# Kernel optimization log

Measured on AMD Instinct MI355X. Metric: run time of the kernel, lower is better.

## Reference

```python
import jax, jax.numpy as jnp
import numpy as np

B, IN, HID, OUT = 1024, 512, 128, 64
INP1 = IN + 1  # 513, after prepending ones column


def setup_inputs() -> dict:
    key = jax.random.key(0)
    k1, k2, k3, k4, k5, k6, k7, k8 = jax.random.split(key, 8)
    s1 = 1.0 / np.sqrt(INP1 * INP1)
    s2 = 1.0 / np.sqrt(HID)
    return {
        "img": jax.random.normal(k1, (B, IN), dtype=jnp.float32),
        "tab": jax.random.normal(k2, (B, IN), dtype=jnp.float32),
        "W1": jax.random.uniform(k3, (HID, INP1 * INP1), jnp.float32, -s1, s1),
        "b1": jax.random.uniform(k4, (HID,), jnp.float32, -s1, s1),
        "W2": jax.random.uniform(k5, (HID, HID), jnp.float32, -s2, s2),
        "b2": jax.random.uniform(k6, (HID,), jnp.float32, -s2, s2),
        "W3": jax.random.uniform(k7, (OUT, HID), jnp.float32, -s2, s2),
        "b3": jax.random.uniform(k8, (OUT,), jnp.float32, -s2, s2),
    }


def reference(img, tab, W1, b1, W2, b2, W3, b3):
    ones = jnp.ones((img.shape[0], 1), dtype=img.dtype)
    x = jnp.concatenate([ones, img], axis=1)  # [B, IN+1]
    t = jnp.concatenate([ones, tab], axis=1)  # [B, IN+1]
    # batched outer product, flattened: [B, (IN+1)*(IN+1)]
    fusion = jnp.einsum("bi,bj->bij", x, t).reshape(x.shape[0], -1)
    # dropout is identity in eval mode
    y1 = fusion @ W1.T + b1
    y2 = jnp.tanh(y1 @ W2.T + b2)
    y3 = jax.nn.relu(y2 @ W3.T + b3)
    return y3
```

## Files before the change

kernel.cpp:

```cpp
#include <hip/hip_runtime.h>
#include <hip/hip_bf16.h>

typedef __bf16 bf16x8 __attribute__((ext_vector_type(8)));
typedef float f32x4 __attribute__((ext_vector_type(4)));

#define B_SZ   1024
#define IN_SZ  512
#define HID    128
#define OUT_SZ 64
#define KPAD   544
#define BM     64
#define BN     512
#define BK     32
#define NKT    (KPAD/BK)
#define APAD   40

static __device__ __forceinline__ unsigned short f2bf(float f) {
    __hip_bfloat16 h = __float2bfloat16(f);
    return *reinterpret_cast<unsigned short*>(&h);
}

__global__ __launch_bounds__(256) void prep_kernel(
    const float* __restrict__ img, const float* __restrict__ tab,
    unsigned short* __restrict__ tbt, float* __restrict__ xhT)
{
    const int blk = blockIdx.x;
    for (int j = threadIdx.x; j < KPAD; j += 256) {
        float v = (j == 0) ? 1.0f : (j < 513 ? tab[(size_t)blk * IN_SZ + (j - 1)] : 0.0f);
        tbt[(size_t)blk * KPAD + j] = f2bf(v);
    }
    if (blk < KPAD) {
        const int i = blk;
        for (int b = threadIdx.x; b < B_SZ; b += 256) {
            float v = (i == 0) ? 1.0f : (i < 513 ? img[(size_t)b * IN_SZ + (i - 1)] : 0.0f);
            xhT[(size_t)i * B_SZ + b] = v;
        }
    }
}

__global__ __launch_bounds__(512) void gemm_fused(
    const float* __restrict__ w1, const unsigned short* __restrict__ tbt,
    const float* __restrict__ xhT, float* __restrict__ y1acc)
{
    __shared__ unsigned short Als[BM][APAD];
    __shared__ unsigned short Bls[BN][APAD];

    const int bm = blockIdx.x >> 1;
    const int bn = blockIdx.x & 1;
    const int m0 = bm * BM;
    const int n0 = bn * BN;
    const int tid  = threadIdx.x;
    const int wv   = tid >> 6;
    const int lane = tid & 63;
    const int l15  = lane & 15;
    const int kg   = lane >> 4;

    const f32x4 zero4 = {0.f, 0.f, 0.f, 0.f};
    f32x4 acc[4][4];
    #pragma unroll
    for (int i = 0; i < 4; ++i)
        #pragma unroll
        for (int j = 0; j < 4; ++j) acc[i][j] = zero4;

    const int ar = tid >> 3;
    const int ac = (tid & 7) << 2;

    for (int kt = 0; kt < NKT; ++kt) {
        __syncthreads();
        {
            const int j0 = kt * BK + ac;
            const size_t gb = (size_t)(m0 + ar) * 513 + j0;
            unsigned short u0, u1, u2, u3;
            if (kt < NKT - 1) {
                u0 = f2bf(w1[gb + 0]); u1 = f2bf(w1[gb + 1]);
                u2 = f2bf(w1[gb + 2]); u3 = f2bf(w1[gb + 3]);
            } else {
                u0 = (j0 + 0 < 513) ? f2bf(w1[gb + 0]) : (unsigned short)0;
                u1 = (j0 + 1 < 513) ? f2bf(w1[gb + 1]) : (unsigned short)0;
                u2 = (j0 + 2 < 513) ? f2bf(w1[gb + 2]) : (unsigned short)0;
                u3 = (j0 + 3 < 513) ? f2bf(w1[gb + 3]) : (unsigned short)0;
            }
            Als[ar][ac + 0] = u0; Als[ar][ac + 1] = u1;
            Als[ar][ac + 2] = u2; Als[ar][ac + 3] = u3;
        }
        {
            const uint4* src = reinterpret_cast<const uint4*>(
                tbt + (size_t)(n0 + tid) * KPAD + kt * BK);
            uint4 v0 = src[0], v1 = src[1], v2 = src[2], v3 = src[3];
            uint4* dst = reinterpret_cast<uint4*>(&Bls[tid][0]);
            dst[0] = v0; dst[1] = v1; dst[2] = v2; dst[3] = v3;
        }
        __syncthreads();
        bf16x8 af[4], bfr[4];
        #pragma unroll
        for (int ms = 0; ms < 4; ++ms)
            af[ms] = *reinterpret_cast<const bf16x8*>(&Als[ms * 16 + l15][kg * 8]);
        #pragma unroll
        for (int ns = 0; ns < 4; ++ns)
            bfr[ns] = *reinterpret_cast<const bf16x8*>(&Bls[wv * 64 + ns * 16 + l15][kg * 8]);
        #pragma unroll
        for (int ms = 0; ms < 4; ++ms)
            #pragma unroll
            for (int ns = 0; ns < 4; ++ns)
                acc[ms][ns] = __builtin_amdgcn_mfma_f32_16x16x32_bf16(
                    af[ms], bfr[ns], acc[ms][ns], 0, 0, 0);
    }

    const int h0 = m0 / 513;
    const int mb = (h0 + 1) * 513;
    const bool cross = (mb < m0 + BM);
    #pragma unroll
    for (int ns = 0; ns < 4; ++ns) {
        const int ncol = n0 + wv * 64 + ns * 16 + l15;
        float s0 = 0.f, s1 = 0.f;
        #pragma unroll
        for (int ms = 0; ms < 4; ++ms) {
            #pragma unroll
            for (int v = 0; v < 4; ++v) {
                const int m = m0 + ms * 16 + kg * 4 + v;
                const bool lo = (m < mb);
                const int i = lo ? (m - h0 * 513) : (m - mb);
                const float xv = xhT[(size_t)i * B_SZ + ncol];
                const float val = acc[ms][ns][v] * xv;
                if (lo) s0 += val; else s1 += val;
            }
        }
        s0 += __shfl_xor(s0, 16); s0 += __shfl_xor(s0, 32);
        if (lane < 16) atomicAdd(&y1acc[(size_t)ncol * HID + h0], s0);
        if (cross) {
            s1 += __shfl_xor(s1, 16); s1 += __shfl_xor(s1, 32);
            if (lane < 16 && (h0 + 1) < HID)
                atomicAdd(&y1acc[(size_t)ncol * HID + h0 + 1], s1);
        }
    }
}

__global__ __launch_bounds__(128) void mlp_kernel(
    const float* __restrict__ y1acc, const float* __restrict__ b1,
    const float* __restrict__ W2, const float* __restrict__ b2,
    const float* __restrict__ W3, const float* __restrict__ b3,
    float* __restrict__ out)
{
    __shared__ float y1r[HID];
    __shared__ float y2r[HID];
    const int b = blockIdx.x;
    const int h = threadIdx.x;
    y1r[h] = y1acc[(size_t)b * HID + h] + b1[h];
    __syncthreads();
    float a = b2[h];
    const float* w2r = W2 + (size_t)h * HID;
    #pragma unroll 8
    for (int k = 0; k < HID; ++k) a += w2r[k] * y1r[k];
    y2r[h] = tanhf(a);
    __syncthreads();
    if (h < OUT_SZ) {
        float a3 = b3[h];
        const float* w3r = W3 + (size_t)h * HID;
        #pragma unroll 8
        for (int k = 0; k < HID; ++k) a3 += w3r[k] * y2r[k];
        out[(size_t)b * OUT_SZ + h] = fmaxf(a3, 0.f);
    }
}

extern "C" void kernel_launch(void* const* d_in, const int* in_sizes, int n_in,
                              void* d_out, int out_size, void* d_ws, size_t ws_size,
                              hipStream_t stream) {
    const float* img = (const float*)d_in[0];
    const float* tab = (const float*)d_in[1];
    const float* W1  = (const float*)d_in[2];
    const float* b1  = (const float*)d_in[3];
    const float* W2  = (const float*)d_in[4];
    const float* b2  = (const float*)d_in[5];
    const float* W3  = (const float*)d_in[6];
    const float* b3  = (const float*)d_in[7];
    float* out = (float*)d_out;

    char* ws = (char*)d_ws;
    float*          y1acc = (float*)ws;
    unsigned short* tbt   = (unsigned short*)(ws + 524288);
    float*          xhT   = (float*)(ws + 524288 + 1114112);

    hipMemsetAsync(y1acc, 0, (size_t)B_SZ * HID * sizeof(float), stream);
    prep_kernel<<<dim3(1024), dim3(256), 0, stream>>>(img, tab, tbt, xhT);
    gemm_fused<<<dim3(2052), dim3(512), 0, stream>>>(W1, tbt, xhT, y1acc);
    mlp_kernel<<<dim3(1024), dim3(128), 0, stream>>>(y1acc, b1, W2, b2, W3, b3, out);
}
```

Baseline: 228.0 us.

## Peel last K column into epilogue, use direct global-to-LDS loads and swizzled LDS

Shrinks the K loop from 17 to 16 tiles of 32 by handling the 513th column (the last tab element times the last W1 column) as a scalar correction in the epilogue. The B tile is now loaded with global_load_lds directly into LDS, and the padded LDS arrays are replaced by unpadded ones with an XOR swizzle to avoid bank conflicts. The A tile is written with one vectorized store per thread, and launch bounds request 4 blocks per CU. The epilogue now does extra strided reads of W1 and reads the new tc buffer, and the prep kernel writes that buffer. The tbt row stride drops from 544 to 512.

Measured after the change: 216.1 us. -5.2%, faster.

```diff
diff --git a/kernel.cpp b/kernel.cpp
--- a/kernel.cpp
+++ b/kernel.cpp
@@ -3,17 +3,20 @@
 
 typedef __bf16 bf16x8 __attribute__((ext_vector_type(8)));
 typedef float f32x4 __attribute__((ext_vector_type(4)));
+typedef unsigned short u16x4 __attribute__((ext_vector_type(4)));
+
+typedef __attribute__((address_space(1))) const unsigned int gu32;
+typedef __attribute__((address_space(3))) unsigned int lu32;
 
 #define B_SZ   1024
 #define IN_SZ  512
 #define HID    128
 #define OUT_SZ 64
-#define KPAD   544
+#define M_TOT  65664
 #define BM     64
 #define BN     512
 #define BK     32
-#define NKT    (KPAD/BK)
-#define APAD   40
+#define NKT    16
 
 static __device__ __forceinline__ unsigned short f2bf(float f) {
     __hip_bfloat16 h = __float2bfloat16(f);
@@ -22,28 +25,29 @@
 
 __global__ __launch_bounds__(256) void prep_kernel(
     const float* __restrict__ img, const float* __restrict__ tab,
-    unsigned short* __restrict__ tbt, float* __restrict__ xhT)
+    unsigned short* __restrict__ tbt, float* __restrict__ xhT,
+    float* __restrict__ tc)
 {
     const int blk = blockIdx.x;
-    for (int j = threadIdx.x; j < KPAD; j += 256) {
-        float v = (j == 0) ? 1.0f : (j < 513 ? tab[(size_t)blk * IN_SZ + (j - 1)] : 0.0f);
-        tbt[(size_t)blk * KPAD + j] = f2bf(v);
-    }
-    if (blk < KPAD) {
-        const int i = blk;
-        for (int b = threadIdx.x; b < B_SZ; b += 256) {
-            float v = (i == 0) ? 1.0f : (i < 513 ? img[(size_t)b * IN_SZ + (i - 1)] : 0.0f);
-            xhT[(size_t)i * B_SZ + b] = v;
-        }
-    }
-}
-
-__global__ __launch_bounds__(512) void gemm_fused(
+    for (int j = threadIdx.x; j < 512; j += 256) {
+        float v = (j == 0) ? 1.0f : tab[(size_t)blk * IN_SZ + (j - 1)];
+        tbt[(size_t)blk * 512 + j] = f2bf(v);
+    }
+    if (threadIdx.x == 0) tc[blk] = tab[(size_t)blk * IN_SZ + 511];
+    if (blk < 513) {
+        for (int b = threadIdx.x; b < B_SZ; b += 256)
+            xhT[(size_t)blk * B_SZ + b] =
+                (blk == 0) ? 1.0f : img[(size_t)b * IN_SZ + (blk - 1)];
+    }
+}
+
+__global__ __launch_bounds__(512, 4) void gemm_fused(
     const float* __restrict__ w1, const unsigned short* __restrict__ tbt,
-    const float* __restrict__ xhT, float* __restrict__ y1acc)
+    const float* __restrict__ xhT, const float* __restrict__ tc,
+    float* __restrict__ y1acc)
 {
-    __shared__ unsigned short Als[BM][APAD];
-    __shared__ unsigned short Bls[BN][APAD];
+    __shared__ unsigned short Als[BM * BK];
+    __shared__ unsigned short Bls[BN * BK];
 
     const int bm = blockIdx.x >> 1;
     const int bn = blockIdx.x & 1;
@@ -55,49 +59,62 @@
     const int l15  = lane & 15;
     const int kg   = lane >> 4;
 
-    const f32x4 zero4 = {0.f, 0.f, 0.f, 0.f};
-    f32x4 acc[4][4];
-    #pragma unroll
-    for (int i = 0; i < 4; ++i)
-        #pragma unroll
-        for (int j = 0; j < 4; ++j) acc[i][j] = zero4;
-
-    const int ar = tid >> 3;
-    const int ac = (tid & 7) << 2;
+    const int ar  = tid >> 3;
+    const int ac4 = tid & 7;
+    const int achunk = (ar << 2) | ((ac4 >> 1) ^ ((ar >> 1) & 3));
+    unsigned short* adst = &Als[achunk * 8 + (ac4 & 1) * 4];
+    const float* asrc = w1 + (size_t)(m0 + ar) * 513 + ac4 * 4;
+
+    const unsigned short* bsrc[4];
+    unsigned short* bdst[4];
+    #pragma unroll
+    for (int q = 0; q < 4; ++q) {
+        const int p  = q * 512 + tid;
+        const int r  = p >> 2;
+        const int cl = (p & 3) ^ ((r >> 1) & 3);
+        bsrc[q] = tbt + (size_t)(n0 + r) * 512 + cl * 8;
+        bdst[q] = &Bls[(q * 512 + wv * 64) * 8];
+    }
+
+    int aoffs[4], boffs[4];
+    #pragma unroll
+    for (int ms = 0; ms < 4; ++ms) {
+        const int row = ms * 16 + l15;
+        aoffs[ms] = ((row << 2) | (kg ^ ((row >> 1) & 3))) * 8;
+    }
+    #pragma unroll
+    for (int ns = 0; ns < 4; ++ns) {
+        const int row = wv * 64 + ns * 16 + l15;
+        boffs[ns] = ((row << 2) | (kg ^ ((row >> 1) & 3))) * 8;
+    }
+
+    f32x4 acc[4][4] = {};
 
     for (int kt = 0; kt < NKT; ++kt) {
+        const int k32 = kt * BK;
         __syncthreads();
+        #pragma unroll
+        for (int q = 0; q < 4; ++q)
+            __builtin_amdgcn_global_load_lds(
+                (gu32*)(const void*)(bsrc[q] + k32),
+                (lu32*)(void*)bdst[q], 16, 0, 0);
         {
-            const int j0 = kt * BK + ac;
-            const size_t gb = (size_t)(m0 + ar) * 513 + j0;
-            unsigned short u0, u1, u2, u3;
-            if (kt < NKT - 1) {
-                u0 = f2bf(w1[gb + 0]); u1 = f2bf(w1[gb + 1]);
-                u2 = f2bf(w1[gb + 2]); u3 = f2bf(w1[gb + 3]);
-            } else {
-                u0 = (j0 + 0 < 513) ? f2bf(w1[gb + 0]) : (unsigned short)0;
-                u1 = (j0 + 1 < 513) ? f2bf(w1[gb + 1]) : (unsigned short)0;
-                u2 = (j0 + 2 < 513) ? f2bf(w1[gb + 2]) : (unsigned short)0;
-                u3 = (j0 + 3 < 513) ? f2bf(w1[gb + 3]) : (unsigned short)0;
-            }
-            Als[ar][ac + 0] = u0; Als[ar][ac + 1] = u1;
-            Als[ar][ac + 2] = u2; Als[ar][ac + 3] = u3;
-        }
-        {
-            const uint4* src = reinterpret_cast<const uint4*>(
-                tbt + (size_t)(n0 + tid) * KPAD + kt * BK);
-            uint4 v0 = src[0], v1 = src[1], v2 = src[2], v3 = src[3];
-            uint4* dst = reinterpret_cast<uint4*>(&Bls[tid][0]);
-            dst[0] = v0; dst[1] = v1; dst[2] = v2; dst[3] = v3;
+            const float f0 = asrc[k32 + 0], f1 = asrc[k32 + 1];
+            const float f2 = asrc[k32 + 2], f3 = asrc[k32 + 3];
+            u16x4 uv;
+            uv[0] = f2bf(f0); uv[1] = f2bf(f1);
+            uv[2] = f2bf(f2); uv[3] = f2bf(f3);
+            *reinterpret_cast<u16x4*>(adst) = uv;
         }
         __syncthreads();
+
         bf16x8 af[4], bfr[4];
         #pragma unroll
         for (int ms = 0; ms < 4; ++ms)
-            af[ms] = *reinterpret_cast<const bf16x8*>(&Als[ms * 16 + l15][kg * 8]);
+            af[ms] = *reinterpret_cast<const bf16x8*>(&Als[aoffs[ms]]);
         #pragma unroll
         for (int ns = 0; ns < 4; ++ns)
-            bfr[ns] = *reinterpret_cast<const bf16x8*>(&Bls[wv * 64 + ns * 16 + l15][kg * 8]);
+            bfr[ns] = *reinterpret_cast<const bf16x8*>(&Bls[boffs[ns]]);
         #pragma unroll
         for (int ms = 0; ms < 4; ++ms)
             #pragma unroll
@@ -109,9 +126,18 @@
     const int h0 = m0 / 513;
     const int mb = (h0 + 1) * 513;
     const bool cross = (mb < m0 + BM);
+
+    float wc[4][4];
+    #pragma unroll
+    for (int ms = 0; ms < 4; ++ms)
+        #pragma unroll
+        for (int v = 0; v < 4; ++v)
+            wc[ms][v] = w1[(size_t)(m0 + ms * 16 + kg * 4 + v) * 513 + 512];
+
     #pragma unroll
     for (int ns = 0; ns < 4; ++ns) {
         const int ncol = n0 + wv * 64 + ns * 16 + l15;
+        const float tv = tc[ncol];
         float s0 = 0.f, s1 = 0.f;
         #pragma unroll
         for (int ms = 0; ms < 4; ++ms) {
@@ -121,7 +147,7 @@
                 const bool lo = (m < mb);
                 const int i = lo ? (m - h0 * 513) : (m - mb);
                 const float xv = xhT[(size_t)i * B_SZ + ncol];
-                const float val = acc[ms][ns][v] * xv;
+                const float val = (acc[ms][ns][v] + wc[ms][v] * tv) * xv;
                 if (lo) s0 += val; else s1 += val;
             }
         }
@@ -178,10 +204,11 @@
     char* ws = (char*)d_ws;
     float*          y1acc = (float*)ws;
     unsigned short* tbt   = (unsigned short*)(ws + 524288);
-    float*          xhT   = (float*)(ws + 524288 + 1114112);
+    float*          xhT   = (float*)(ws + 1572864);
+    float*          tc    = (float*)(ws + 3674112);
 
     hipMemsetAsync(y1acc, 0, (size_t)B_SZ * HID * sizeof(float), stream);
-    prep_kernel<<<dim3(1024), dim3(256), 0, stream>>>(img, tab, tbt, xhT);
-    gemm_fused<<<dim3(2052), dim3(512), 0, stream>>>(W1, tbt, xhT, y1acc);
+    prep_kernel<<<dim3(1024), dim3(256), 0, stream>>>(img, tab, tbt, xhT, tc);
+    gemm_fused<<<dim3(2052), dim3(512), 0, stream>>>(W1, tbt, xhT, tc, y1acc);
     mlp_kernel<<<dim3(1024), dim3(128), 0, stream>>>(y1acc, b1, W2, b2, W3, b3, out);
 }
```
